# Performance work log

Hardware: AMD Instinct MI355X
Metric: run time of the kernel (lower is better)

## Reference

```python
import jax, jax.numpy as jnp
import numpy as np

B, N, DIM, H, DH = 8, 4096, 512, 8, 64
M = 266  # nb_features = int(dim_head * ln(dim_head)) = int(64*4.1589)
LN_EPS = 1e-5
K_EPS = 1e-4  # performer softmax_kernel epsilon


def _gaussian_orthogonal_matrix(m, d, rng):
    # performer_pytorch default: stacked QR blocks, rows scaled by chi(d) norms
    blocks = []
    n_full = m // d
    for _ in range(n_full):
        q, _ = np.linalg.qr(rng.standard_normal((d, d)))
        blocks.append(q.T)
    rem = m - n_full * d
    if rem > 0:
        q, _ = np.linalg.qr(rng.standard_normal((d, d)))
        blocks.append(q.T[:rem])
    proj = np.concatenate(blocks, axis=0)
    norms = np.linalg.norm(rng.standard_normal((m, d)), axis=1)
    return (proj * norms[:, None]).astype(np.float32)


def setup_inputs() -> dict:
    key = jax.random.key(0)
    ks = jax.random.split(key, 8)
    s_in = 1.0 / np.sqrt(DIM)
    s_ff = 1.0 / np.sqrt(4 * DIM)
    rng = np.random.default_rng(0)
    return {
        "x": jax.random.normal(ks[0], (B, N, DIM), jnp.float32),
        "w_q": jax.random.normal(ks[1], (DIM, DIM), jnp.float32) * s_in,
        "w_k": jax.random.normal(ks[2], (DIM, DIM), jnp.float32) * s_in,
        "w_v": jax.random.normal(ks[3], (DIM, DIM), jnp.float32) * s_in,
        "w_o": jax.random.normal(ks[4], (DIM, DIM), jnp.float32) * s_in,
        "b_o": jnp.zeros((DIM,), jnp.float32),
        "ln1_g": jnp.ones((DIM,), jnp.float32),
        "ln1_b": jnp.zeros((DIM,), jnp.float32),
        "ln2_g": jnp.ones((DIM,), jnp.float32),
        "ln2_b": jnp.zeros((DIM,), jnp.float32),
        "ff_w1": jax.random.normal(ks[5], (DIM, 4 * DIM), jnp.float32) * s_in,
        "ff_b1": jnp.zeros((4 * DIM,), jnp.float32),
        "ff_w2": jax.random.normal(ks[6], (4 * DIM, DIM), jnp.float32) * s_ff,
        "ff_b2": jnp.zeros((DIM,), jnp.float32),
        "projection": jnp.asarray(_gaussian_orthogonal_matrix(M, DH, rng)),
    }


def _layernorm(x, g, b):
    mu = jnp.mean(x, -1, keepdims=True)
    var = jnp.mean((x - mu) ** 2, -1, keepdims=True)
    return (x - mu) * jax.lax.rsqrt(var + LN_EPS) * g + b


def _softmax_kernel(data, proj, is_query):
    # FAVOR+ positive softmax-kernel features (performer_pytorch.softmax_kernel)
    dn = data.shape[-1] ** -0.25  # data_normalizer
    ratio = proj.shape[0] ** -0.5
    dd = jnp.einsum("bhnd,md->bhnm", data * dn, proj)
    diag = jnp.sum(data ** 2, -1, keepdims=True) * 0.5 * (dn ** 2)  # [B,H,N,1]
    if is_query:
        mx = jax.lax.stop_gradient(jnp.max(dd, -1, keepdims=True))
    else:
        mx = jax.lax.stop_gradient(jnp.max(dd))
    return ratio * (jnp.exp(dd - diag - mx) + K_EPS)


def reference(x, w_q, w_k, w_v, w_o, b_o, ln1_g, ln1_b, ln2_g, ln2_b,
              ff_w1, ff_b1, ff_w2, ff_b2, projection):
    # --- attention sublayer (pre-norm) ---
    h = _layernorm(x, ln1_g, ln1_b)

    def split_heads(t):
        return t.reshape(B, N, H, DH).transpose(0, 2, 1, 3)  # [B,H,N,DH]

    q = split_heads(h @ w_q)
    k = split_heads(h @ w_k)
    v = split_heads(h @ w_v)

    qp = _softmax_kernel(q, projection, True)   # [B,H,N,M]
    kp = _softmax_kernel(k, projection, False)  # [B,H,N,M]

    # non-causal linear attention: O(N) in sequence length
    d_inv = 1.0 / jnp.einsum("bhnm,bhm->bhn", qp, jnp.sum(kp, axis=2))
    ctx = jnp.einsum("bhnm,bhnd->bhmd", kp, v)          # [B,H,M,DH]
    attn = jnp.einsum("bhnm,bhmd,bhn->bhnd", qp, ctx, d_inv)
    attn = attn.transpose(0, 2, 1, 3).reshape(B, N, DIM)
    x = x + attn @ w_o + b_o

    # --- feed-forward sublayer (pre-norm) ---
    h2 = _layernorm(x, ln2_g, ln2_b)
    ff = jax.nn.gelu(h2 @ ff_w1 + ff_b1, approximate=False) @ ff_w2 + ff_b2
    return x + ff
```

## Files before the change

kernel.cpp:

```cpp
#include <hip/hip_runtime.h>
#include <cmath>

typedef unsigned short u16;
typedef unsigned int u32;
typedef short bf16x8 __attribute__((ext_vector_type(8)));
typedef float f32x4 __attribute__((ext_vector_type(4)));

#define DEVI __device__ __forceinline__

constexpr int NSEQ = 4096, DIMM = 512;
constexpr int KVLD = 1024;
constexpr int MP = 288;
constexpr int MPP = 296;
constexpr int MREAL = 266;
constexpr int DHP = 96;
constexpr float LNEPS = 1e-5f;
constexpr float KEPS = 1e-4f;
constexpr float DN = 0.3535533905932738f;
constexpr float HALF_DN2 = 0.0625f;

DEVI u16 f2bf(float f) {
  u32 u = __float_as_uint(f);
  u32 r = (u + 0x7FFFu + ((u >> 16) & 1u)) >> 16;
  return (u16)r;
}
DEVI float bf2f(u16 h) { return __uint_as_float(((u32)h) << 16); }

DEVI f32x4 mfma16(bf16x8 a, bf16x8 b, f32x4 c) {
  return __builtin_amdgcn_mfma_f32_16x16x32_bf16(a, b, c, 0, 0, 0);
}

DEVI void gload_lds16(const void* g, void* l) {
  __builtin_amdgcn_global_load_lds(
      (const __attribute__((address_space(1))) u32*)g,
      (__attribute__((address_space(3))) u32*)l, 16, 0, 0);
}

DEVI float gelu_fast(float z) {
  float a = fminf(1.5957691216057308f * (z + 0.044715f * z * z * z), 60.f);
  float e = __expf(a);
  return z * e * __builtin_amdgcn_rcpf(e + 1.f);
}

__global__ void ws_sentinel(float* out) { out[0] = 12345.0f; }

__launch_bounds__(256)
__global__ void transpose_cvt(const float* __restrict__ in, u16* __restrict__ out,
                              int K, int Nn) {
  __shared__ float tl[32][33];
  int ntn = Nn >> 5;
  int bid = blockIdx.x;
  int kt = bid / ntn, ntt = bid - kt * ntn;
  int k0 = kt << 5, nn0 = ntt << 5;
  int t = threadIdx.x;
  int r = t >> 5, c = t & 31;
#pragma unroll
  for (int i = 0; i < 4; ++i)
    tl[r + i * 8][c] = in[(size_t)(k0 + r + i * 8) * Nn + nn0 + c];
  __syncthreads();
#pragma unroll
  for (int i = 0; i < 4; ++i)
    out[(size_t)(nn0 + r + i * 8) * K + k0 + c] = f2bf(tl[c][r + i * 8]);
}

__global__ void proj_prep(const float* __restrict__ proj, u16* __restrict__ projf) {
  int idx = blockIdx.x * 256 + threadIdx.x;
  if (idx >= MP * 64) return;
  int e = idx & 7, lane = (idx >> 3) & 63, fh = idx >> 9;
  int f = fh >> 1, half = fh & 1;
  int m = f * 16 + (lane & 15);
  int d = half * 32 + (lane >> 4) * 8 + e;
  float v = (m < MREAL) ? proj[m * 64 + d] * DN : 0.f;
  projf[idx] = f2bf(v);
}

__launch_bounds__(256)
__global__ void ln_fwd(const float* __restrict__ x, const float* __restrict__ g,
                       const float* __restrict__ bt, u16* __restrict__ out) {
  int w = threadIdx.x >> 6, lane = threadIdx.x & 63;
  int row = blockIdx.x * 4 + w;
  const float* xr = x + (size_t)row * DIMM;
  int c0 = lane * 4;
  float4 v0 = *(const float4*)(xr + c0);
  float4 v1 = *(const float4*)(xr + 256 + c0);
  float s = v0.x + v0.y + v0.z + v0.w + v1.x + v1.y + v1.z + v1.w;
  float sq = v0.x * v0.x + v0.y * v0.y + v0.z * v0.z + v0.w * v0.w +
             v1.x * v1.x + v1.y * v1.y + v1.z * v1.z + v1.w * v1.w;
#pragma unroll
  for (int mk = 1; mk < 64; mk <<= 1) {
    s += __shfl_xor(s, mk, 64);
    sq += __shfl_xor(sq, mk, 64);
  }
  float mu = s * (1.f / 512.f);
  float var = sq * (1.f / 512.f) - mu * mu;
  float rstd = rsqrtf(var + LNEPS);
  float4 g0 = *(const float4*)(g + c0);
  float4 g1 = *(const float4*)(g + 256 + c0);
  float4 b0 = *(const float4*)(bt + c0);
  float4 b1 = *(const float4*)(bt + 256 + c0);
  u16* orow = out + (size_t)row * DIMM;
  uint2 p0, p1;
  {
    u16 h0 = f2bf((v0.x - mu) * rstd * g0.x + b0.x);
    u16 h1 = f2bf((v0.y - mu) * rstd * g0.y + b0.y);
    u16 h2 = f2bf((v0.z - mu) * rstd * g0.z + b0.z);
    u16 h3 = f2bf((v0.w - mu) * rstd * g0.w + b0.w);
    p0.x = ((u32)h1 << 16) | h0; p0.y = ((u32)h3 << 16) | h2;
  }
  {
    u16 h0 = f2bf((v1.x - mu) * rstd * g1.x + b1.x);
    u16 h1 = f2bf((v1.y - mu) * rstd * g1.y + b1.y);
    u16 h2 = f2bf((v1.z - mu) * rstd * g1.z + b1.z);
    u16 h3 = f2bf((v1.w - mu) * rstd * g1.w + b1.w);
    p1.x = ((u32)h1 << 16) | h0; p1.y = ((u32)h3 << 16) | h2;
  }
  *(uint2*)(orow + c0) = p0;
  *(uint2*)(orow + 256 + c0) = p1;
}

#define WAITVM(N) asm volatile("s_waitcnt vmcnt(" #N ")" ::: "memory")

template <int EPI>
__launch_bounds__(512)
__global__ void gemm256(const u16* __restrict__ A, int lda,
                        const u16* __restrict__ Bt, int ldb, int K,
                        void* __restrict__ OutP, int Nout, int ldo,
                        const float* __restrict__ bias,
                        const float* __restrict__ Res) {
  __shared__ __align__(16) u16 Al[2][256 * 64];
  __shared__ __align__(16) u16 Bl[2][256 * 64];
  int ntiles = Nout >> 8;
  int nwg = gridDim.x;
  int bid = blockIdx.x;
  int cpx = nwg >> 3;
  int wg = (bid & 7) * cpx + (bid >> 3);
  int mt = wg / ntiles, nt = wg - mt * ntiles;
  int t = threadIdx.x, lane = t & 63, w = t >> 6;
  int wm = w >> 2, wn = w & 3;
  int fr = lane & 15, fq = lane >> 4;
  int rowA0 = mt * 256, colB0 = nt * 256;
  int swz = (fr & 7) << 4;

  f32x4 acc[8][4];
#pragma unroll
  for (int i = 0; i < 8; ++i)
#pragma unroll
    for (int j = 0; j < 4; ++j) acc[i][j] = f32x4{0.f, 0.f, 0.f, 0.f};

  int srow = t >> 3;
  int so = ((t * 16) & 127) ^ ((srow & 7) << 4);

#define STAGE_G(bufi, k0)                                                       \
  do {                                                                          \
    _Pragma("unroll") for (int it = 0; it < 4; ++it) {                          \
      gload_lds16(                                                              \
          (const char*)(A + ((size_t)(rowA0 + srow + it * 64) * lda + (k0))) + so, \
          (char*)Al[bufi] + t * 16 + it * 8192);                                \
      gload_lds16(                                                              \
          (const char*)(Bt + ((size_t)(colB0 + srow + it * 64) * ldb + (k0))) + so, \
          (char*)Bl[bufi] + t * 16 + it * 8192);                                \
    }                                                                           \
  } while (0)

  int NT = K >> 6;
  STAGE_G(0, 0);
  STAGE_G(1, 64);
  int bi = 0;
  for (int tt = 0; tt < NT; ++tt) {
    if (tt + 1 < NT) { WAITVM(8); } else { WAITVM(0); }
    __builtin_amdgcn_s_barrier();

    bf16x8 av[8][2], bv[4][2];
#pragma unroll
    for (int i = 0; i < 8; ++i)
#pragma unroll
      for (int ks = 0; ks < 2; ++ks) {
        int row = wm * 128 + i * 16 + fr;
        av[i][ks] = *(const bf16x8*)((const char*)Al[bi] + row * 128 +
                                     (((ks << 6) | (fq << 4)) ^ swz));
      }
#pragma unroll
    for (int j = 0; j < 4; ++j)
#pragma unroll
      for (int ks = 0; ks < 2; ++ks) {
        int row = wn * 64 + (j)*16 + fr;
        bv[j][ks] = *(const bf16x8*)((const char*)Bl[bi] + row * 128 +
                                     (((ks << 6) | (fq << 4)) ^ swz));
      }

    __builtin_amdgcn_s_setprio(1);
#pragma unroll
    for (int i = 0; i < 4; ++i)
#pragma unroll
      for (int j = 0; j < 4; ++j)
#pragma unroll
        for (int ks = 0; ks < 2; ++ks)
          acc[i][j] = mfma16(av[i][ks], bv[j][ks], acc[i][j]);
    __builtin_amdgcn_s_setprio(0);

    asm volatile("s_waitcnt lgkmcnt(0)" ::: "memory");
    __builtin_amdgcn_sched_barrier(0);
    __builtin_amdgcn_s_barrier();
    if (tt + 2 < NT) STAGE_G(bi, (tt + 2) * 64);

    __builtin_amdgcn_s_setprio(1);
#pragma unroll
    for (int i = 4; i < 8; ++i)
#pragma unroll
      for (int j = 0; j < 4; ++j)
#pragma unroll
        for (int ks = 0; ks < 2; ++ks)
          acc[i][j] = mfma16(av[i][ks], bv[j][ks], acc[i][j]);
    __builtin_amdgcn_s_setprio(0);
    bi ^= 1;
  }
#undef STAGE_G

#pragma unroll
  for (int i = 0; i < 8; ++i)
#pragma unroll
    for (int j = 0; j < 4; ++j) {
      int row = rowA0 + wm * 128 + i * 16 + fq * 4;
      int col = colB0 + wn * 64 + j * 16 + fr;
#pragma unroll
      for (int r = 0; r < 4; ++r) {
        float v = acc[i][j][r];
        size_t idx = (size_t)(row + r) * ldo + col;
        if constexpr (EPI == 0) {
          ((u16*)OutP)[idx] = f2bf(v);
        } else if constexpr (EPI == 1) {
          ((float*)OutP)[idx] = v + bias[col] + Res[(size_t)(row + r) * 512 + col];
        } else if constexpr (EPI == 2) {
          ((u16*)OutP)[idx] = f2bf(gelu_fast(v + bias[col]));
        } else {
          float bb = bias ? bias[col] : 0.f;
          ((float*)OutP)[idx] += v + bb;
        }
      }
    }
}

__launch_bounds__(256)
__global__ void kmax_kernel(const u16* __restrict__ kv, const u16* __restrict__ projf,
                            u32* __restrict__ maxslot) {
  __shared__ float wred[4];
  int bid = blockIdx.x;
  int bh = bid >> 6, nt = bid & 63;
  int b = bh >> 3, h = bh & 7;
  int n0 = nt * 64;
  int t = threadIdx.x, lane = t & 63, w = t >> 6;
  int fr = lane & 15, fq = lane >> 4;

  const u16* krow = kv + ((size_t)(b * NSEQ + n0 + w * 16 + fr)) * KVLD + h * 64;
  bf16x8 a0 = *(const bf16x8*)(krow + fq * 8);
  bf16x8 a1 = *(const bf16x8*)(krow + 32 + fq * 8);

  const bf16x8* pf = (const bf16x8*)projf;
  float m = -1e30f;
#pragma unroll
  for (int f = 0; f < 18; ++f) {
    bf16x8 b0 = pf[(f * 2 + 0) * 64 + lane];
    bf16x8 b1 = pf[(f * 2 + 1) * 64 + lane];
    f32x4 z = {0.f, 0.f, 0.f, 0.f};
    z = mfma16(a0, b0, z);
    z = mfma16(a1, b1, z);
    if (f * 16 + fr < MREAL) {
#pragma unroll
      for (int r = 0; r < 4; ++r) m = fmaxf(m, z[r]);
    }
  }
#pragma unroll
  for (int mk = 1; mk < 64; mk <<= 1) m = fmaxf(m, __shfl_xor(m, mk, 64));
  if (lane == 0) wred[w] = m;
  __syncthreads();
  if (t == 0) {
    float mm = fmaxf(fmaxf(wred[0], wred[1]), fmaxf(wred[2], wred[3]));
    u32 u = __float_as_uint(mm);
    u32 enc = (u & 0x80000000u) ? ~u : (u | 0x80000000u);
    atomicMax(maxslot, enc);
  }
}

__launch_bounds__(512)
__global__ void fused_ctx(const u16* __restrict__ kvbuf, const u16* __restrict__ projf,
                          const u32* __restrict__ maxslot, float* __restrict__ part) {
  __shared__ __align__(16) u16 kt[2][64 * 64];
  __shared__ __align__(16) u16 kpL[MP * 64];
  __shared__ __align__(16) u16 vL[DHP * 64];
  int bid = blockIdx.x;
  int bh = bid >> 2, s = bid & 3;
  int b = bh >> 3, h = bh & 7;
  int t = threadIdx.x, lane = t & 63, w = t >> 6;
  int fr = lane & 15, fq = lane >> 4;
  int rg = w & 3, fh = w >> 2;
  int wq4 = w >> 1, wn = w & 1;
  int i_base = (wq4 < 2) ? wq4 * 5 : 10 + (wq4 - 2) * 4;
  int i_cnt = (wq4 < 2) ? 5 : 4;

  if (t < 256) {
    int rr = 64 + (t >> 3), sg = t & 7;
    u16 val = (rr == 64) ? (u16)0x3F80 : (u16)0;
    uint4 v4; u16* pv = (u16*)&v4;
#pragma unroll
    for (int e = 0; e < 8; ++e) pv[e] = val;
    *(uint4*)(vL + rr * 64 + sg * 8) = v4;
  }
  u32 enc = *maxslot;
  float gmax = __uint_as_float((enc & 0x80000000u) ? (enc & 0x7FFFFFFFu) : ~enc);
  const bf16x8* pf = (const bf16x8*)projf;

  bf16x8 pfr0[9], pfr1[9];
#pragma unroll
  for (int ff = 0; ff < 9; ++ff) {
    pfr0[ff] = pf[((fh * 9 + ff) * 2 + 0) * 64 + lane];
    pfr1[ff] = pf[((fh * 9 + ff) * 2 + 1) * 64 + lane];
  }

  f32x4 acc[5][3];
#pragma unroll
  for (int i = 0; i < 5; ++i)
#pragma unroll
    for (int j = 0; j < 3; ++j) acc[i][j] = f32x4{0.f, 0.f, 0.f, 0.f};

  int str = t >> 3;
  int sch = (t & 7) ^ (str & 7);
  int vr0 = t >> 4, vsg = t & 15;
  uint2 vra, vrb;

#define KT_LOAD(ci, n0)                                                        \
  gload_lds16(kvbuf + ((size_t)(b * NSEQ + (n0) + str)) * KVLD + h * 64 + sch * 8, \
              (char*)kt[ci] + t * 16)
#define V_LOAD(n0)                                                             \
  do {                                                                         \
    vra = *(const uint2*)(kvbuf + ((size_t)(b * NSEQ + (n0) + vr0)) * KVLD + 512 + h * 64 + vsg * 4); \
    vrb = *(const uint2*)(kvbuf + ((size_t)(b * NSEQ + (n0) + vr0 + 32)) * KVLD + 512 + h * 64 + vsg * 4); \
  } while (0)

  KT_LOAD(0, s * 1024);
  V_LOAD(s * 1024);
  int cur = 0;

  for (int tile = 0; tile < 16; ++tile) {
    int n0 = s * 1024 + tile * 64;
    WAITVM(0);

    {
      u16* pv = (u16*)&vra;
#pragma unroll
      for (int e = 0; e < 4; ++e) {
        int d = vsg * 4 + e, ch = (vr0 >> 3) ^ (d & 7);
        ((u16*)((char*)vL + d * 128 + ch * 16))[vr0 & 7] = pv[e];
      }
      u16* pw = (u16*)&vrb;
      int r2 = vr0 + 32;
#pragma unroll
      for (int e = 0; e < 4; ++e) {
        int d = vsg * 4 + e, ch = (r2 >> 3) ^ (d & 7);
        ((u16*)((char*)vL + d * 128 + ch * 16))[r2 & 7] = pw[e];
      }
    }
    if (tile < 15) { KT_LOAD(cur ^ 1, n0 + 64); V_LOAD(n0 + 64); }
    asm volatile("s_waitcnt lgkmcnt(0)" ::: "memory");
    __builtin_amdgcn_s_barrier();

    int rowa = rg * 16 + fr;
    bf16x8 a0 = *(const bf16x8*)((const char*)kt[cur] + rowa * 128 +
                                 ((fq ^ (fr & 7)) << 4));
    bf16x8 a1 = *(const bf16x8*)((const char*)kt[cur] + rowa * 128 +
                                 (((4 + fq) ^ (fr & 7)) << 4));

    float ss = 0.f;
#pragma unroll
    for (int e = 0; e < 8; ++e) {
      float x0 = bf2f((u16)a0[e]), x1 = bf2f((u16)a1[e]);
      ss += x0 * x0 + x1 * x1;
    }
    ss += __shfl_xor(ss, 16, 64);
    ss += __shfl_xor(ss, 32, 64);
    float dgv[4];
#pragma unroll
    for (int r4 = 0; r4 < 4; ++r4)
      dgv[r4] = __shfl(ss, fq * 4 + r4, 64) * HALF_DN2;

#pragma unroll
    for (int ff = 0; ff < 9; ++ff) {
      int f = fh * 9 + ff;
      f32x4 z = {0.f, 0.f, 0.f, 0.f};
      z = mfma16(a0, pfr0[ff], z);
      z = mfma16(a1, pfr1[ff], z);
      int col = f * 16 + fr;
      bool ok = col < MREAL;
      float k0v = ok ? (__expf(z[0] - dgv[0] - gmax) + KEPS) : 0.f;
      float k1v = ok ? (__expf(z[1] - dgv[1] - gmax) + KEPS) : 0.f;
      float k2v = ok ? (__expf(z[2] - dgv[2] - gmax) + KEPS) : 0.f;
      float k3v = ok ? (__expf(z[3] - dgv[3] - gmax) + KEPS) : 0.f;
      u32 lo, hi;
      asm("v_cvt_pk_bf16_f32 %0, %1, %2" : "=v"(lo) : "v"(k0v), "v"(k1v));
      asm("v_cvt_pk_bf16_f32 %0, %1, %2" : "=v"(hi) : "v"(k2v), "v"(k3v));
      uint2 pk2; pk2.x = lo; pk2.y = hi;
      int ch = (rg * 2 + (fq >> 1)) ^ (fr & 7);
      *(uint2*)((char*)kpL + col * 128 + ch * 16 + (fq & 1) * 8) = pk2;
    }
    asm volatile("s_waitcnt lgkmcnt(0)" ::: "memory");
    __builtin_amdgcn_s_barrier();

#pragma unroll
    for (int kc = 0; kc < 2; ++kc) {
      int rch = ((kc * 4 + fq) ^ (fr & 7)) << 4;
      bf16x8 av[5], bv[3];
#pragma unroll
      for (int i = 0; i < 5; ++i)
        if (i < i_cnt)
          av[i] = *(const bf16x8*)((const char*)kpL + ((i_base + i) * 16 + fr) * 128 + rch);
#pragma unroll
      for (int j = 0; j < 3; ++j)
        bv[j] = *(const bf16x8*)((const char*)vL + (wn * 48 + j * 16 + fr) * 128 + rch);
#pragma unroll
      for (int i = 0; i < 5; ++i)
        if (i < i_cnt)
#pragma unroll
          for (int j = 0; j < 3; ++j) acc[i][j] = mfma16(av[i], bv[j], acc[i][j]);
    }
    asm volatile("s_waitcnt lgkmcnt(0)" ::: "memory");
    __builtin_amdgcn_s_barrier();
    cur ^= 1;
  }
#undef KT_LOAD
#undef V_LOAD

  float* dst = part + ((size_t)bh * 4 + s) * MP * DHP;
#pragma unroll
  for (int i = 0; i < 5; ++i)
    if (i < i_cnt)
#pragma unroll
      for (int j = 0; j < 3; ++j) {
        int m = (i_base + i) * 16 + fq * 4;
        int c = wn * 48 + j * 16 + fr;
#pragma unroll
        for (int r = 0; r < 4; ++r) dst[(size_t)(m + r) * DHP + c] = acc[i][j][r];
      }
}

__launch_bounds__(256)
__global__ void ctx_reduce2(const float* __restrict__ part, u16* __restrict__ ctxT) {
  int bh = blockIdx.x, t = threadIdx.x;
  const float* p = part + (size_t)bh * 4 * MP * DHP;
  u16* dst = ctxT + (size_t)bh * DHP * MP;
  for (int idx = t; idx < DHP * MP; idx += 256) {
    int d = idx / MP, m = idx - d * MP;
    size_t o = (size_t)m * DHP + d;
    float v = p[o] + p[o + MP * DHP] + p[o + 2 * MP * DHP] + p[o + 3 * MP * DHP];
    dst[idx] = f2bf(v);
  }
}

__launch_bounds__(256)
__global__ void fused_attn(const u16* __restrict__ qb, const u16* __restrict__ ctxT,
                           const u16* __restrict__ projf, u16* __restrict__ attnb) {
  __shared__ __align__(16) u16 qt[64 * 64];
  __shared__ __align__(16) u16 qpL[64 * MPP];
  __shared__ float dbuf[64];
  int bid = blockIdx.x;
  int bh = bid >> 6, nt = bid & 63;
  int b = bh >> 3, h = bh & 7;
  int n0 = nt * 64;
  int t = threadIdx.x, lane = t & 63, w = t >> 6;
  int wm = w >> 1, wn = w & 1;
  int fr = lane & 15, fq = lane >> 4;

#pragma unroll
  for (int it = 0; it < 4; ++it) {
    int idx = t + it * 256;
    int r = idx >> 4, sg = idx & 15;
    int dst = (r * 128 + sg * 8) ^ ((r & 7) << 4);
    *(uint2*)((char*)qt + dst) =
        *(const uint2*)(qb + ((size_t)(b * NSEQ + n0 + r)) * KVLD + h * 64 + sg * 4);
  }
  __syncthreads();

  int swz = (fr & 7) << 4;
  bf16x8 a0 = *(const bf16x8*)((const char*)qt +
                               (((w * 16 + fr) * 128 + fq * 16) ^ swz));
  bf16x8 a1 = *(const bf16x8*)((const char*)qt +
                               (((w * 16 + fr) * 128 + 64 + fq * 16) ^ swz));

  float ss = 0.f;
#pragma unroll
  for (int e = 0; e < 8; ++e) {
    float x0 = bf2f((u16)a0[e]), x1 = bf2f((u16)a1[e]);
    ss += x0 * x0 + x1 * x1;
  }
  ss += __shfl_xor(ss, 16, 64);
  ss += __shfl_xor(ss, 32, 64);
  float dg = ss * HALF_DN2;

  const bf16x8* pf = (const bf16x8*)projf;
  f32x4 accf[18];
#pragma unroll
  for (int f = 0; f < 18; ++f) {
    f32x4 z = {0.f, 0.f, 0.f, 0.f};
    z = mfma16(pf[(f * 2 + 0) * 64 + lane], a0, z);
    z = mfma16(pf[(f * 2 + 1) * 64 + lane], a1, z);
    accf[f] = z;
  }
  float mm = -1e30f;
#pragma unroll
  for (int f = 0; f < 18; ++f)
#pragma unroll
    for (int r = 0; r < 4; ++r) mm = fmaxf(mm, accf[f][r]);
  mm = fmaxf(mm, __shfl_xor(mm, 16, 64));
  mm = fmaxf(mm, __shfl_xor(mm, 32, 64));

  u16* qp = qpL + (w * 16 + fr) * MPP + fq * 4;
#pragma unroll
  for (int f = 0; f < 18; ++f) {
    float e0 = __expf(accf[f][0] - dg - mm) + KEPS;
    float e1 = __expf(accf[f][1] - dg - mm) + KEPS;
    float e2 = __expf(accf[f][2] - dg - mm) + KEPS;
    float e3 = __expf(accf[f][3] - dg - mm) + KEPS;
    u32 lo, hi;
    asm("v_cvt_pk_bf16_f32 %0, %1, %2" : "=v"(lo) : "v"(e0), "v"(e1));
    asm("v_cvt_pk_bf16_f32 %0, %1, %2" : "=v"(hi) : "v"(e2), "v"(e3));
    uint2 pk; pk.x = lo; pk.y = hi;
    *(uint2*)(qp + f * 16) = pk;
  }
  __syncthreads();

  const u16* cg = ctxT + (size_t)bh * DHP * MP;
  f32x4 acc2[2][3];
#pragma unroll
  for (int i = 0; i < 2; ++i)
#pragma unroll
    for (int j = 0; j < 3; ++j) acc2[i][j] = f32x4{0.f, 0.f, 0.f, 0.f};
  bf16x8 bvc[3];
#pragma unroll
  for (int j = 0; j < 3; ++j)
    bvc[j] = *(const bf16x8*)(cg + (size_t)(wn * 48 + j * 16 + fr) * MP + fq * 8);
#pragma unroll
  for (int kc = 0; kc < 9; ++kc) {
    bf16x8 bvn[3];
    if (kc < 8) {
#pragma unroll
      for (int j = 0; j < 3; ++j)
        bvn[j] = *(const bf16x8*)(cg + (size_t)(wn * 48 + j * 16 + fr) * MP +
                                  (kc + 1) * 32 + fq * 8);
    }
    bf16x8 av[2];
#pragma unroll
    for (int i = 0; i < 2; ++i)
      av[i] = *(const bf16x8*)(qpL + (wm * 32 + i * 16 + fr) * MPP + kc * 32 + fq * 8);
#pragma unroll
    for (int i = 0; i < 2; ++i)
#pragma unroll
      for (int j = 0; j < 3; ++j) acc2[i][j] = mfma16(av[i], bvc[j], acc2[i][j]);
    if (kc < 8) {
#pragma unroll
      for (int j = 0; j < 3; ++j) bvc[j] = bvn[j];
    }
  }
  if (wn == 1 && fr == 0) {
#pragma unroll
    for (int i = 0; i < 2; ++i) {
      int rl = wm * 32 + i * 16 + fq * 4;
#pragma unroll
      for (int r = 0; r < 4; ++r) dbuf[rl + r] = acc2[i][1][r];
    }
  }
  __syncthreads();

  u16* ob = qt;
#pragma unroll
  for (int i = 0; i < 2; ++i)
#pragma unroll
    for (int j = 0; j < 3; ++j) {
      int cl = wn * 48 + j * 16 + fr;
      if (cl < 64) {
        int rl = wm * 32 + i * 16 + fq * 4;
#pragma unroll
        for (int r = 0; r < 4; ++r)
          ob[(rl + r) * 64 + cl] = f2bf(acc2[i][j][r] / dbuf[rl + r]);
      }
    }
  __syncthreads();

  u16* dst = attnb + ((size_t)(b * NSEQ + n0)) * KVLD + h * 64;
  for (int idx = t; idx < 64 * 8; idx += 256) {
    int r = idx >> 3, sg = idx & 7;
    *(uint4*)(dst + (size_t)r * KVLD + sg * 8) = *(const uint4*)(ob + r * 64 + sg * 8);
  }
}

constexpr size_t OFF_WQT   = 0;
constexpr size_t OFF_WKT   = 524288;
constexpr size_t OFF_WVT   = 1048576;
constexpr size_t OFF_WOT   = 1572864;
constexpr size_t OFF_FF1T  = 2097152;
constexpr size_t OFF_FF2T  = 4194304;
constexpr size_t OFF_PROJF = 6328320;
constexpr size_t OFF_MAX   = 6365184;
constexpr size_t OFF_CTXT  = 6365440;
constexpr size_t OFF_H     = 9904384;
constexpr size_t OFF_KV    = 43458816;
constexpr size_t OFF_PART  = 110567680;
constexpr size_t WS_NEED   = 138879232;

extern "C" void kernel_launch(void* const* d_in, const int* in_sizes, int n_in,
                              void* d_out, int out_size, void* d_ws, size_t ws_size,
                              hipStream_t stream) {
  const float* x    = (const float*)d_in[0];
  const float* w_q  = (const float*)d_in[1];
  const float* w_k  = (const float*)d_in[2];
  const float* w_v  = (const float*)d_in[3];
  const float* w_o  = (const float*)d_in[4];
  const float* b_o  = (const float*)d_in[5];
  const float* ln1g = (const float*)d_in[6];
  const float* ln1b = (const float*)d_in[7];
  const float* ln2g = (const float*)d_in[8];
  const float* ln2b = (const float*)d_in[9];
  const float* ffw1 = (const float*)d_in[10];
  const float* ffb1 = (const float*)d_in[11];
  const float* ffw2 = (const float*)d_in[12];
  const float* ffb2 = (const float*)d_in[13];
  const float* proj = (const float*)d_in[14];
  (void)in_sizes; (void)n_in; (void)out_size;

  float* dout = (float*)d_out;
  if (ws_size < WS_NEED) {
    ws_sentinel<<<1, 1, 0, stream>>>(dout);
    return;
  }

  char* ws = (char*)d_ws;
  u16* wqt   = (u16*)(ws + OFF_WQT);
  u16* wkt   = (u16*)(ws + OFF_WKT);
  u16* wvt   = (u16*)(ws + OFF_WVT);
  u16* wot   = (u16*)(ws + OFF_WOT);
  u16* ff1t  = (u16*)(ws + OFF_FF1T);
  u16* ff2t  = (u16*)(ws + OFF_FF2T);
  u16* projf = (u16*)(ws + OFF_PROJF);
  u32* maxsl = (u32*)(ws + OFF_MAX);
  u16* ctxt  = (u16*)(ws + OFF_CTXT);
  u16* hbuf  = (u16*)(ws + OFF_H);
  u16* kvbuf = (u16*)(ws + OFF_KV);
  float* part = (float*)(ws + OFF_PART);

  hipMemsetAsync(maxsl, 0, 4, stream);

  transpose_cvt<<<256, 256, 0, stream>>>(w_q, wqt, 512, 512);
  transpose_cvt<<<256, 256, 0, stream>>>(w_k, wkt, 512, 512);
  transpose_cvt<<<256, 256, 0, stream>>>(w_v, wvt, 512, 512);
  transpose_cvt<<<256, 256, 0, stream>>>(w_o, wot, 512, 512);
  transpose_cvt<<<1024, 256, 0, stream>>>(ffw1, ff1t, 512, 2048);
  transpose_cvt<<<1024, 256, 0, stream>>>(ffw2, ff2t, 2048, 512);
  proj_prep<<<72, 256, 0, stream>>>(proj, projf);

  ln_fwd<<<8192, 256, 0, stream>>>(x, ln1g, ln1b, hbuf);
  gemm256<0><<<512, 512, 0, stream>>>(hbuf, 512, wkt, 512, 512, kvbuf, 1024, 1024, nullptr, nullptr);
  kmax_kernel<<<4096, 256, 0, stream>>>(kvbuf, projf, maxsl);
  fused_ctx<<<256, 512, 0, stream>>>(kvbuf, projf, maxsl, part);
  ctx_reduce2<<<64, 256, 0, stream>>>(part, ctxt);
  gemm256<0><<<256, 512, 0, stream>>>(hbuf, 512, wqt, 512, 512, kvbuf, 512, 1024, nullptr, nullptr);
  fused_attn<<<4096, 256, 0, stream>>>(kvbuf, ctxt, projf, kvbuf + 512);
  gemm256<1><<<256, 512, 0, stream>>>(kvbuf + 512, 1024, wot, 512, 512, dout, 512, 512, b_o, x);
  ln_fwd<<<8192, 256, 0, stream>>>(dout, ln2g, ln2b, hbuf);
  for (int c = 0; c < 2; ++c) {
    gemm256<2><<<512, 512, 0, stream>>>(hbuf, 512, ff1t + (size_t)c * 1024 * 512, 512, 512,
                                        kvbuf, 1024, 1024, ffb1 + c * 1024, nullptr);
    gemm256<3><<<256, 512, 0, stream>>>(kvbuf, 1024, ff2t + c * 1024, 2048, 1024,
                                        dout, 512, 512, (c == 0) ? ffb2 : nullptr, nullptr);
  }
}
```

Measured before the change: 601.2 us.

## Split GEMM main loop into four quadrant phases with separate A/B staging

```diff
diff --git a/kernel.cpp b/kernel.cpp
--- a/kernel.cpp
+++ b/kernel.cpp
@@ -150,12 +150,17 @@
   int srow = t >> 3;
   int so = ((t * 16) & 127) ^ ((srow & 7) << 4);
 
-#define STAGE_G(bufi, k0)                                                       \
+#define STAGE_A(bufi, k0)                                                       \
   do {                                                                          \
     _Pragma("unroll") for (int it = 0; it < 4; ++it) {                          \
       gload_lds16(                                                              \
           (const char*)(A + ((size_t)(rowA0 + srow + it * 64) * lda + (k0))) + so, \
           (char*)Al[bufi] + t * 16 + it * 8192);                                \
+    }                                                                           \
+  } while (0)
+#define STAGE_B(bufi, k0)                                                       \
+  do {                                                                          \
+    _Pragma("unroll") for (int it = 0; it < 4; ++it) {                          \
       gload_lds16(                                                              \
           (const char*)(Bt + ((size_t)(colB0 + srow + it * 64) * ldb + (k0))) + so, \
           (char*)Bl[bufi] + t * 16 + it * 8192);                                \
@@ -163,16 +168,18 @@
   } while (0)
 
   int NT = K >> 6;
-  STAGE_G(0, 0);
-  STAGE_G(1, 64);
+  STAGE_A(0, 0);
+  STAGE_B(0, 0);
+  STAGE_A(1, 64);
+  STAGE_B(1, 64);
   int bi = 0;
   for (int tt = 0; tt < NT; ++tt) {
     if (tt + 1 < NT) { WAITVM(8); } else { WAITVM(0); }
     __builtin_amdgcn_s_barrier();
 
-    bf16x8 av[8][2], bv[4][2];
-#pragma unroll
-    for (int i = 0; i < 8; ++i)
+    bf16x8 av[4][2], bv[4][2];
+#pragma unroll
+    for (int i = 0; i < 4; ++i)
 #pragma unroll
       for (int ks = 0; ks < 2; ++ks) {
         int row = wm * 128 + i * 16 + fr;
@@ -180,41 +187,81 @@
                                      (((ks << 6) | (fq << 4)) ^ swz));
       }
 #pragma unroll
-    for (int j = 0; j < 4; ++j)
+    for (int j = 0; j < 2; ++j)
 #pragma unroll
       for (int ks = 0; ks < 2; ++ks) {
-        int row = wn * 64 + (j)*16 + fr;
+        int row = wn * 64 + j * 16 + fr;
         bv[j][ks] = *(const bf16x8*)((const char*)Bl[bi] + row * 128 +
                                      (((ks << 6) | (fq << 4)) ^ swz));
       }
-
     __builtin_amdgcn_s_setprio(1);
 #pragma unroll
     for (int i = 0; i < 4; ++i)
 #pragma unroll
-      for (int j = 0; j < 4; ++j)
+      for (int j = 0; j < 2; ++j)
 #pragma unroll
         for (int ks = 0; ks < 2; ++ks)
           acc[i][j] = mfma16(av[i][ks], bv[j][ks], acc[i][j]);
     __builtin_amdgcn_s_setprio(0);
-
+    __builtin_amdgcn_s_barrier();
+
+#pragma unroll
+    for (int j = 2; j < 4; ++j)
+#pragma unroll
+      for (int ks = 0; ks < 2; ++ks) {
+        int row = wn * 64 + j * 16 + fr;
+        bv[j][ks] = *(const bf16x8*)((const char*)Bl[bi] + row * 128 +
+                                     (((ks << 6) | (fq << 4)) ^ swz));
+      }
+    __builtin_amdgcn_s_setprio(1);
+#pragma unroll
+    for (int i = 0; i < 4; ++i)
+#pragma unroll
+      for (int j = 2; j < 4; ++j)
+#pragma unroll
+        for (int ks = 0; ks < 2; ++ks)
+          acc[i][j] = mfma16(av[i][ks], bv[j][ks], acc[i][j]);
+    __builtin_amdgcn_s_setprio(0);
     asm volatile("s_waitcnt lgkmcnt(0)" ::: "memory");
     __builtin_amdgcn_sched_barrier(0);
     __builtin_amdgcn_s_barrier();
-    if (tt + 2 < NT) STAGE_G(bi, (tt + 2) * 64);
-
+    if (tt + 2 < NT) STAGE_B(bi, (tt + 2) * 64);
+
+#pragma unroll
+    for (int i = 0; i < 4; ++i)
+#pragma unroll
+      for (int ks = 0; ks < 2; ++ks) {
+        int row = wm * 128 + (i + 4) * 16 + fr;
+        av[i][ks] = *(const bf16x8*)((const char*)Al[bi] + row * 128 +
+                                     (((ks << 6) | (fq << 4)) ^ swz));
+      }
     __builtin_amdgcn_s_setprio(1);
 #pragma unroll
-    for (int i = 4; i < 8; ++i)
-#pragma unroll
-      for (int j = 0; j < 4; ++j)
+    for (int i = 0; i < 4; ++i)
+#pragma unroll
+      for (int j = 0; j < 2; ++j)
 #pragma unroll
         for (int ks = 0; ks < 2; ++ks)
-          acc[i][j] = mfma16(av[i][ks], bv[j][ks], acc[i][j]);
+          acc[i + 4][j] = mfma16(av[i][ks], bv[j][ks], acc[i + 4][j]);
+    __builtin_amdgcn_s_setprio(0);
+    asm volatile("s_waitcnt lgkmcnt(0)" ::: "memory");
+    __builtin_amdgcn_sched_barrier(0);
+    __builtin_amdgcn_s_barrier();
+    if (tt + 2 < NT) STAGE_A(bi, (tt + 2) * 64);
+
+    __builtin_amdgcn_s_setprio(1);
+#pragma unroll
+    for (int i = 0; i < 4; ++i)
+#pragma unroll
+      for (int j = 2; j < 4; ++j)
+#pragma unroll
+        for (int ks = 0; ks < 2; ++ks)
+          acc[i + 4][j] = mfma16(av[i][ks], bv[j][ks], acc[i + 4][j]);
     __builtin_amdgcn_s_setprio(0);
     bi ^= 1;
   }
-#undef STAGE_G
+#undef STAGE_A
+#undef STAGE_B
 
 #pragma unroll
   for (int i = 0; i < 8; ++i)
```

Measured after the change: 604.0 us. About the same (+0.5%).

## Fuse FFN up-projection, GELU and down-projection into one kernel

Applied to the files above, without the earlier changes.

```diff
diff --git a/kernel.cpp b/kernel.cpp
--- a/kernel.cpp
+++ b/kernel.cpp
@@ -72,6 +72,24 @@
   int d = half * 32 + (lane >> 4) * 8 + e;
   float v = (m < MREAL) ? proj[m * 64 + d] * DN : 0.f;
   projf[idx] = f2bf(v);
+}
+
+__global__ void w1_prep(const float* __restrict__ w1, u16* __restrict__ w1f) {
+  int idx = blockIdx.x * 256 + threadIdx.x;
+  int e = idx & 7, lane = (idx >> 3) & 63;
+  int k16 = (idx >> 9) & 15, hcf = idx >> 13;
+  int hcol = hcf * 16 + (lane & 15);
+  int k = k16 * 32 + (lane >> 4) * 8 + e;
+  w1f[idx] = f2bf(w1[(size_t)k * 2048 + hcol]);
+}
+
+__global__ void w2_prep(const float* __restrict__ w2, u16* __restrict__ w2f) {
+  int idx = blockIdx.x * 256 + threadIdx.x;
+  int e = idx & 7, lane = (idx >> 3) & 63;
+  int hk16 = (idx >> 9) & 63, ocf = idx >> 15;
+  int ocol = ocf * 16 + (lane & 15);
+  int hk = hk16 * 32 + (lane >> 4) * 8 + e;
+  w2f[idx] = f2bf(w2[(size_t)hk * 512 + ocol]);
 }
 
 __launch_bounds__(256)
@@ -228,15 +246,110 @@
         size_t idx = (size_t)(row + r) * ldo + col;
         if constexpr (EPI == 0) {
           ((u16*)OutP)[idx] = f2bf(v);
-        } else if constexpr (EPI == 1) {
+        } else {
           ((float*)OutP)[idx] = v + bias[col] + Res[(size_t)(row + r) * 512 + col];
-        } else if constexpr (EPI == 2) {
-          ((u16*)OutP)[idx] = f2bf(gelu_fast(v + bias[col]));
-        } else {
-          float bb = bias ? bias[col] : 0.f;
-          ((float*)OutP)[idx] += v + bb;
         }
       }
+    }
+}
+
+__launch_bounds__(512)
+__global__ void ffn_fused(const u16* __restrict__ hb, const u16* __restrict__ w1f,
+                          const u16* __restrict__ w2f, const float* __restrict__ b1,
+                          const float* __restrict__ b2, float* __restrict__ dout) {
+  __shared__ __align__(16) u16 As[128 * 512];
+  __shared__ __align__(16) u16 hS[128 * 64];
+  int nwg = gridDim.x;
+  int bid = blockIdx.x;
+  int cpx = nwg >> 3;
+  int wg = (bid & 7) * cpx + (bid >> 3);
+  int row0 = wg * 128;
+  int t = threadIdx.x, lane = t & 63, w = t >> 6;
+  int fr = lane & 15, fq = lane >> 4;
+  int hcolf = w & 3, rh = w >> 2;
+  int oc0 = w * 64;
+
+#pragma unroll
+  for (int it = 0; it < 16; ++it) {
+    int L = t + it * 512;
+    int r = L >> 6, pc = L & 63;
+    int lc = pc ^ (r & 7);
+    gload_lds16(hb + ((size_t)(row0 + r)) * 512 + lc * 8, (char*)As + L * 16);
+  }
+
+  f32x4 acc2[8][4];
+#pragma unroll
+  for (int i = 0; i < 8; ++i)
+#pragma unroll
+    for (int j = 0; j < 4; ++j) acc2[i][j] = f32x4{0.f, 0.f, 0.f, 0.f};
+
+  WAITVM(0);
+  __syncthreads();
+
+  for (int ch = 0; ch < 32; ++ch) {
+    f32x4 acch[4];
+#pragma unroll
+    for (int i = 0; i < 4; ++i) acch[i] = f32x4{0.f, 0.f, 0.f, 0.f};
+    const u16* w1p = w1f + ((size_t)(ch * 4 + hcolf) * 16) * 512 + lane * 8;
+#pragma unroll
+    for (int kk = 0; kk < 16; ++kk) {
+      bf16x8 av = *(const bf16x8*)(w1p + kk * 512);
+#pragma unroll
+      for (int i = 0; i < 4; ++i) {
+        int r = rh * 64 + i * 16 + fr;
+        bf16x8 bv = *(const bf16x8*)((const char*)As + r * 1024 +
+                                     (((kk * 4 + fq) ^ (r & 7)) << 4));
+        acch[i] = mfma16(av, bv, acch[i]);
+      }
+    }
+    float bb0 = b1[ch * 64 + hcolf * 16 + fq * 4 + 0];
+    float bb1 = b1[ch * 64 + hcolf * 16 + fq * 4 + 1];
+    float bb2 = b1[ch * 64 + hcolf * 16 + fq * 4 + 2];
+    float bb3 = b1[ch * 64 + hcolf * 16 + fq * 4 + 3];
+#pragma unroll
+    for (int i = 0; i < 4; ++i) {
+      int arow = rh * 64 + i * 16 + fr;
+      float g0 = gelu_fast(acch[i][0] + bb0);
+      float g1 = gelu_fast(acch[i][1] + bb1);
+      float g2 = gelu_fast(acch[i][2] + bb2);
+      float g3 = gelu_fast(acch[i][3] + bb3);
+      u32 lo, hi;
+      asm("v_cvt_pk_bf16_f32 %0, %1, %2" : "=v"(lo) : "v"(g0), "v"(g1));
+      asm("v_cvt_pk_bf16_f32 %0, %1, %2" : "=v"(hi) : "v"(g2), "v"(g3));
+      uint2 pk; pk.x = lo; pk.y = hi;
+      int cl = hcolf * 2 + (fq >> 1);
+      *(uint2*)((char*)hS + arow * 128 + ((cl ^ (arow & 7)) << 4) + (fq & 1) * 8) = pk;
+    }
+    __syncthreads();
+
+#pragma unroll
+    for (int k16 = 0; k16 < 2; ++k16) {
+      bf16x8 bw[4];
+#pragma unroll
+      for (int j = 0; j < 4; ++j)
+        bw[j] = *(const bf16x8*)(w2f +
+                 ((size_t)((w * 4 + j) * 64 + ch * 2 + k16)) * 512 + lane * 8);
+#pragma unroll
+      for (int i = 0; i < 8; ++i) {
+        int r = i * 16 + fr;
+        bf16x8 ah = *(const bf16x8*)((const char*)hS + r * 128 +
+                                     (((k16 * 4 + fq) ^ (r & 7)) << 4));
+#pragma unroll
+        for (int j = 0; j < 4; ++j) acc2[i][j] = mfma16(ah, bw[j], acc2[i][j]);
+      }
+    }
+    __syncthreads();
+  }
+
+#pragma unroll
+  for (int i = 0; i < 8; ++i)
+#pragma unroll
+    for (int j = 0; j < 4; ++j) {
+      int row = row0 + i * 16 + fq * 4;
+      int col = oc0 + j * 16 + fr;
+#pragma unroll
+      for (int r = 0; r < 4; ++r)
+        dout[(size_t)(row + r) * 512 + col] += acc2[i][j][r] + b2[col];
     }
 }
 
@@ -594,8 +707,8 @@
 constexpr size_t OFF_WKT   = 524288;
 constexpr size_t OFF_WVT   = 1048576;
 constexpr size_t OFF_WOT   = 1572864;
-constexpr size_t OFF_FF1T  = 2097152;
-constexpr size_t OFF_FF2T  = 4194304;
+constexpr size_t OFF_W1F   = 2097152;
+constexpr size_t OFF_W2F   = 4194304;
 constexpr size_t OFF_PROJF = 6328320;
 constexpr size_t OFF_MAX   = 6365184;
 constexpr size_t OFF_CTXT  = 6365440;
@@ -635,8 +748,8 @@
   u16* wkt   = (u16*)(ws + OFF_WKT);
   u16* wvt   = (u16*)(ws + OFF_WVT);
   u16* wot   = (u16*)(ws + OFF_WOT);
-  u16* ff1t  = (u16*)(ws + OFF_FF1T);
-  u16* ff2t  = (u16*)(ws + OFF_FF2T);
+  u16* w1f   = (u16*)(ws + OFF_W1F);
+  u16* w2f   = (u16*)(ws + OFF_W2F);
   u16* projf = (u16*)(ws + OFF_PROJF);
   u32* maxsl = (u32*)(ws + OFF_MAX);
   u16* ctxt  = (u16*)(ws + OFF_CTXT);
@@ -650,8 +763,8 @@
   transpose_cvt<<<256, 256, 0, stream>>>(w_k, wkt, 512, 512);
   transpose_cvt<<<256, 256, 0, stream>>>(w_v, wvt, 512, 512);
   transpose_cvt<<<256, 256, 0, stream>>>(w_o, wot, 512, 512);
-  transpose_cvt<<<1024, 256, 0, stream>>>(ffw1, ff1t, 512, 2048);
-  transpose_cvt<<<1024, 256, 0, stream>>>(ffw2, ff2t, 2048, 512);
+  w1_prep<<<4096, 256, 0, stream>>>(ffw1, w1f);
+  w2_prep<<<4096, 256, 0, stream>>>(ffw2, w2f);
   proj_prep<<<72, 256, 0, stream>>>(proj, projf);
 
   ln_fwd<<<8192, 256, 0, stream>>>(x, ln1g, ln1b, hbuf);
@@ -663,10 +776,5 @@
   fused_attn<<<4096, 256, 0, stream>>>(kvbuf, ctxt, projf, kvbuf + 512);
   gemm256<1><<<256, 512, 0, stream>>>(kvbuf + 512, 1024, wot, 512, 512, dout, 512, 512, b_o, x);
   ln_fwd<<<8192, 256, 0, stream>>>(dout, ln2g, ln2b, hbuf);
-  for (int c = 0; c < 2; ++c) {
-    gemm256<2><<<512, 512, 0, stream>>>(hbuf, 512, ff1t + (size_t)c * 1024 * 512, 512, 512,
-                                        kvbuf, 1024, 1024, ffb1 + c * 1024, nullptr);
-    gemm256<3><<<256, 512, 0, stream>>>(kvbuf, 1024, ff2t + c * 1024, 2048, 1024,
-                                        dout, 512, 512, (c == 0) ? ffb2 : nullptr, nullptr);
-  }
-}
+  ffn_fused<<<256, 512, 0, stream>>>(hbuf, w1f, w2f, ffb1, ffb2, dout);
+}
```

Result: slower. 613.3 us (+2.0%).
